# Optimization experiments

Measured on AMD Instinct MI355X. Metric: run time of the kernel, lower is better.

## Reference

```python
import jax, jax.numpy as jnp
import numpy as np

IN_SHAPE_DOWN = (8, 16, 8)   # prod = 1024
OUT_SHAPE_DOWN = (4, 4, 4)   # prod = 64
TT_RANK = 8


def tt_to_dense(cores, in_shape, out_shape):
    """Contract TT-matrix cores [r_{k-1}, i_k, j_k, r_k] into a dense (prod_in, prod_out) matrix."""
    res = cores[0]  # [1, i1, j1, r1]
    for c in cores[1:]:
        res = jnp.einsum('...a,aijb->...ijb', res, c)
    res = res[0, ..., 0]  # (i1, j1, i2, j2, ..., id, jd)
    d = len(in_shape)
    perm = [2 * k for k in range(d)] + [2 * k + 1 for k in range(d)]
    return res.transpose(perm).reshape(int(np.prod(in_shape)), int(np.prod(out_shape)))


def setup_inputs() -> dict:
    key = jax.random.key(0)
    ks = jax.random.split(key, 8)
    r = TT_RANK
    # down cores: in factors (8,16,8) -> out factors (4,4,4)
    d1 = 0.1 * jax.random.normal(ks[0], (1, 8, 4, r), dtype=jnp.float32)
    d2 = 0.1 * jax.random.normal(ks[1], (r, 16, 4, r), dtype=jnp.float32)
    d3 = 0.1 * jax.random.normal(ks[2], (r, 8, 4, 1), dtype=jnp.float32)
    # up cores: shape = [reversed(out_down), reversed(in_down)] = [(4,4,4),(8,16,8)]
    u1 = 0.1 * jax.random.normal(ks[3], (1, 4, 8, r), dtype=jnp.float32)
    u2 = 0.1 * jax.random.normal(ks[4], (r, 4, 16, r), dtype=jnp.float32)
    u3 = 0.1 * jax.random.normal(ks[5], (r, 4, 8, 1), dtype=jnp.float32)
    x = jax.random.normal(ks[6], (4, 4096, 1024), dtype=jnp.float32)
    bias_down = 0.001 * jnp.ones((64,), dtype=jnp.float32)
    bias_up = 0.001 * jnp.ones((1024,), dtype=jnp.float32)
    return {"x": x, "d1": d1, "d2": d2, "d3": d3,
            "u1": u1, "u2": u2, "u3": u3,
            "bias_down": bias_down, "bias_up": bias_up}


def reference(x, d1, d2, d3, u1, u2, u3, bias_down, bias_up):
    # Down-project TT matrix: 1024 -> 64
    Wd = tt_to_dense([d1, d2, d3], IN_SHAPE_DOWN, OUT_SHAPE_DOWN)
    # Up-project TT matrix: 64 -> 1024 (reversed factor shapes)
    Wu = tt_to_dense([u1, u2, u3], tuple(reversed(OUT_SHAPE_DOWN)), tuple(reversed(IN_SHAPE_DOWN)))
    z = jnp.einsum('bsd,dk->bsk', x, Wd) + bias_down
    z = jax.nn.relu(z)
    y = jnp.einsum('bsk,kd->bsd', z, Wu) + bias_up
    return y
```

## Files before the change

kernel.cpp:

```cpp
#include <hip/hip_runtime.h>

typedef float f32x2 __attribute__((ext_vector_type(2)));
typedef float f32x4 __attribute__((ext_vector_type(4)));
typedef short short8 __attribute__((ext_vector_type(8)));

static __device__ __forceinline__ unsigned short f2bf(float f) {
    __bf16 h = (__bf16)f;
    return __builtin_bit_cast(unsigned short, h);
}

static __device__ __forceinline__ void gload_lds16(const void* g, void* l) {
    __builtin_amdgcn_global_load_lds(
        (const __attribute__((address_space(1))) void*)g,
        (__attribute__((address_space(3))) void*)l, 16, 0, 0);
}

__global__ __launch_bounds__(256) void tt_build_w_kernel(
    const float* __restrict__ d1, const float* __restrict__ d2, const float* __restrict__ d3,
    const float* __restrict__ u1, const float* __restrict__ u2, const float* __restrict__ u3,
    unsigned short* __restrict__ WdT_sw, unsigned short* __restrict__ WuT_sw)
{
    int t = blockIdx.x * 256 + threadIdx.x;
    if (t < 65536) {
        int j = t >> 10, i = t & 1023;
        int i1 = i >> 7, i2 = (i >> 3) & 15, i3 = i & 7;
        int j1 = j >> 4, j2 = (j >> 2) & 3, j3 = j & 3;
        float t3[8];
#pragma unroll
        for (int b = 0; b < 8; ++b) t3[b] = d3[(b * 8 + i3) * 4 + j3];
        float wsum = 0.f;
#pragma unroll
        for (int a = 0; a < 8; ++a) {
            float va = d1[(i1 * 4 + j1) * 8 + a];
            const float* p2 = d2 + ((a * 16 + i2) * 4 + j2) * 8;
            float wa = 0.f;
#pragma unroll
            for (int b = 0; b < 8; ++b) wa = fmaf(p2[b], t3[b], wa);
            wsum = fmaf(va, wa, wsum);
        }
        int q_ = i >> 8, ck = (i >> 6) & 3, ks2 = (i >> 5) & 1;
        int kg_ = (i >> 3) & 3, m = i & 7;
        int off = (q_ * 4 + ck) * 4096 + ((ks2 * 4 + kg_) * 64 + j) * 8 + m;
        WdT_sw[off] = f2bf(wsum);
    } else {
        int t2 = t - 65536;
        int d = t2 >> 6, k = t2 & 63;
        int k1 = k >> 4, k2 = (k >> 2) & 3, k3 = k & 3;
        int o1 = d >> 7, o2 = (d >> 3) & 15, o3 = d & 7;
        float t3[8];
#pragma unroll
        for (int b = 0; b < 8; ++b) t3[b] = u3[(b * 4 + k3) * 8 + o3];
        float wsum = 0.f;
#pragma unroll
        for (int a = 0; a < 8; ++a) {
            float va = u1[(k1 * 8 + o1) * 8 + a];
            const float* p2 = u2 + ((a * 4 + k2) * 16 + o2) * 8;
            float wa = 0.f;
#pragma unroll
            for (int b = 0; b < 8; ++b) wa = fmaf(p2[b], t3[b], wa);
            wsum = fmaf(va, wa, wsum);
        }
        int dl = d & 511, hf = d >> 9;
        int off = hf * 32768 + (dl * 8 + ((k >> 3) ^ (dl & 7))) * 8 + (k & 7);
        WuT_sw[off] = f2bf(wsum);
    }
}

__global__ __launch_bounds__(512) void tt_gemm1_kernel(
    const float* __restrict__ x, const unsigned short* __restrict__ WdT_sw,
    const float* __restrict__ bd, unsigned short* __restrict__ zbuf)
{
    extern __shared__ unsigned short wlds[];
    const int t = threadIdx.x;
    const int lane = t & 63;
    const int w = t >> 6;
    const int p = w >> 2;
    const int h = w & 3;
    const int l15 = lane & 15;
    const int kg = lane >> 4;
    const int tile0 = blockIdx.x * 4;

    const int uq = (t & 127) * 2;
    const int tl = t >> 7;
    const int colz = (uq >> 6) * 16 + (uq & 15);
    const int rowz = ((uq & 63) >> 4) * 4;
    const f32x2 bdv = *reinterpret_cast<const f32x2*>(bd + colz);

    {
        const unsigned short* src = WdT_sw + (h * 4 + 2 * p) * 4096 + lane * 8;
        unsigned short* dst = wlds + h * 16384 + 2 * p * 4096;
#pragma unroll
        for (int i = 0; i < 16; ++i)
            gload_lds16(src + i * 512, dst + i * 512);
    }

    const float* xp0 = x + ((size_t)(tile0 + 2 * p) * 16 + l15) * 1024 + h * 256 + kg * 8;
    const float* xp1 = xp0 + 16 * 1024;
    const unsigned short* lb = wlds + h * 16384;

    f32x4 xa[8], xb[8];
#define XL8(D, o0, o1, o2, o3)                                                                     \
    asm volatile("global_load_dwordx4 %0, %1, off offset:" #o0 : "=v"(D[0]) : "v"(xp0) : "memory"); \
    asm volatile("global_load_dwordx4 %0, %1, off offset:" #o1 : "=v"(D[1]) : "v"(xp0) : "memory"); \
    asm volatile("global_load_dwordx4 %0, %1, off offset:" #o2 : "=v"(D[2]) : "v"(xp0) : "memory"); \
    asm volatile("global_load_dwordx4 %0, %1, off offset:" #o3 : "=v"(D[3]) : "v"(xp0) : "memory"); \
    asm volatile("global_load_dwordx4 %0, %1, off offset:" #o0 : "=v"(D[4]) : "v"(xp1) : "memory"); \
    asm volatile("global_load_dwordx4 %0, %1, off offset:" #o1 : "=v"(D[5]) : "v"(xp1) : "memory"); \
    asm volatile("global_load_dwordx4 %0, %1, off offset:" #o2 : "=v"(D[6]) : "v"(xp1) : "memory"); \
    asm volatile("global_load_dwordx4 %0, %1, off offset:" #o3 : "=v"(D[7]) : "v"(xp1) : "memory");

    XL8(xa, 0, 16, 128, 144)
    asm volatile("s_waitcnt vmcnt(8)" ::: "memory");
    __syncthreads();

    f32x4 acc0[4] = {{0.f, 0.f, 0.f, 0.f}, {0.f, 0.f, 0.f, 0.f},
                     {0.f, 0.f, 0.f, 0.f}, {0.f, 0.f, 0.f, 0.f}};
    f32x4 acc1[4] = {{0.f, 0.f, 0.f, 0.f}, {0.f, 0.f, 0.f, 0.f},
                     {0.f, 0.f, 0.f, 0.f}, {0.f, 0.f, 0.f, 0.f}};

#define CPT(XS, CKOFF, WN) do {                                                             \
    asm volatile("s_waitcnt vmcnt(" #WN ")" ::: "memory");                                  \
    __builtin_amdgcn_sched_barrier(0);                                                      \
    const unsigned short* lb_ = lb + CKOFF;                                                 \
    _Pragma("unroll")                                                                       \
    for (int ks2 = 0; ks2 < 2; ++ks2) {                                                     \
        union { short8 v; unsigned short e[8]; } a0, a1;                                    \
        _Pragma("unroll")                                                                   \
        for (int e = 0; e < 4; ++e) {                                                       \
            a0.e[e] = f2bf(XS[ks2 * 2][e]);     a0.e[e + 4] = f2bf(XS[ks2 * 2 + 1][e]);     \
            a1.e[e] = f2bf(XS[4 + ks2 * 2][e]); a1.e[e + 4] = f2bf(XS[4 + ks2 * 2 + 1][e]); \
        }                                                                                   \
        _Pragma("unroll")                                                                   \
        for (int ct = 0; ct < 4; ++ct) {                                                    \
            short8 bf = *reinterpret_cast<const short8*>(                                   \
                lb_ + (ks2 * 4 + kg) * 512 + ct * 128 + l15 * 8);                           \
            acc0[ct] = __builtin_amdgcn_mfma_f32_16x16x32_bf16(a0.v, bf, acc0[ct], 0, 0, 0); \
            acc1[ct] = __builtin_amdgcn_mfma_f32_16x16x32_bf16(a1.v, bf, acc1[ct], 0, 0, 0); \
        }                                                                                   \
    }                                                                                       \
    __builtin_amdgcn_sched_barrier(0);                                                      \
} while (0)

    XL8(xb, 256, 272, 384, 400)
    CPT(xa, 0, 8);
    XL8(xa, 512, 528, 640, 656)
    CPT(xb, 4096, 8);
    XL8(xb, 768, 784, 896, 912)
    CPT(xa, 8192, 8);
    CPT(xb, 12288, 0);
#undef XL8
#undef CPT

    __syncthreads();

    float* red = reinterpret_cast<float*>(wlds);
    {
        float* rp = red + p * 8192 + h * 2048;
#pragma unroll
        for (int ct = 0; ct < 4; ++ct) {
            *reinterpret_cast<f32x4*>(rp + ct * 256 + lane * 4) = acc0[ct];
            *reinterpret_cast<f32x4*>(rp + 1024 + ct * 256 + lane * 4) = acc1[ct];
        }
    }
    __syncthreads();

    {
        const int pp = tl >> 1, tp = tl & 1;
        const float* base = red + pp * 8192 + tp * 1024 + uq * 4;
        f32x4 s0 = {0.f, 0.f, 0.f, 0.f}, s1 = {0.f, 0.f, 0.f, 0.f};
#pragma unroll
        for (int hh = 0; hh < 4; ++hh) {
            f32x4 v0 = *reinterpret_cast<const f32x4*>(base + hh * 2048);
            f32x4 v1 = *reinterpret_cast<const f32x4*>(base + hh * 2048 + 4);
#pragma unroll
            for (int r = 0; r < 4; ++r) { s0[r] += v0[r]; s1[r] += v1[r]; }
        }
        const int tile = tile0 + tl;
#pragma unroll
        for (int r = 0; r < 4; ++r) {
            float z0 = s0[r] + bdv[0]; z0 = z0 > 0.f ? z0 : 0.f;
            float z1 = s1[r] + bdv[1]; z1 = z1 > 0.f ? z1 : 0.f;
            unsigned int pk = (unsigned int)f2bf(z0) | ((unsigned int)f2bf(z1) << 16);
            *reinterpret_cast<unsigned int*>(zbuf + tile * 1024 + (rowz + r) * 64 + colz) = pk;
        }
    }
}

__global__ __launch_bounds__(256) void tt_gemm2_kernel(
    const unsigned short* __restrict__ zbuf, const unsigned short* __restrict__ WuT_sw,
    const float* __restrict__ bu, float* __restrict__ y)
{
    __shared__ unsigned short wlds2[32768];
    const int t = threadIdx.x;
    const int lane = t & 63;
    const int w = t >> 6;
    const int l15 = lane & 15;
    const int kg = lane >> 4;
    const int ch = blockIdx.x & 1;
    const int rg = blockIdx.x >> 1;

    const unsigned short* src = WuT_sw + ch * 32768 + w * 8192 + lane * 8;
#pragma unroll
    for (int i = 0; i < 16; ++i)
        gload_lds16(src + i * 512, &wlds2[w * 8192 + i * 512]);

    f32x4 bv[8];
#pragma unroll
    for (int i = 0; i < 8; ++i)
        bv[i] = *reinterpret_cast<const f32x4*>(bu + ch * 512 + w * 128 + i * 16 + kg * 4);
    __syncthreads();

#pragma unroll
    for (int tt = 0; tt < 8; ++tt) {
        const int tile = rg * 8 + tt;
        short8 az0 = *reinterpret_cast<const short8*>(zbuf + tile * 1024 + l15 * 64 + kg * 8);
        short8 az1 = *reinterpret_cast<const short8*>(zbuf + tile * 1024 + l15 * 64 + 32 + kg * 8);
        const size_t yb = (size_t)(tile * 16 + l15) * 1024 + ch * 512 + w * 128;
#pragma unroll
        for (int i = 0; i < 8; ++i) {
            const int row = w * 128 + i * 16 + l15;
            const int s = row & 7;
            short8 b0 = *reinterpret_cast<const short8*>(&wlds2[(row * 8 + (kg ^ s)) * 8]);
            short8 b1 = *reinterpret_cast<const short8*>(&wlds2[(row * 8 + ((kg + 4) ^ s)) * 8]);
            f32x4 c = {0.f, 0.f, 0.f, 0.f};
            c = __builtin_amdgcn_mfma_f32_16x16x32_bf16(b0, az0, c, 0, 0, 0);
            c = __builtin_amdgcn_mfma_f32_16x16x32_bf16(b1, az1, c, 0, 0, 0);
            f32x4 o;
#pragma unroll
            for (int r = 0; r < 4; ++r) o[r] = c[r] + bv[i][r];
            *reinterpret_cast<f32x4*>(y + yb + i * 16 + kg * 4) = o;
        }
    }
}

extern "C" void kernel_launch(void* const* d_in, const int* in_sizes, int n_in,
                              void* d_out, int out_size, void* d_ws, size_t ws_size,
                              hipStream_t stream) {
    const float* x  = (const float*)d_in[0];
    const float* d1 = (const float*)d_in[1];
    const float* d2 = (const float*)d_in[2];
    const float* d3 = (const float*)d_in[3];
    const float* u1 = (const float*)d_in[4];
    const float* u2 = (const float*)d_in[5];
    const float* u3 = (const float*)d_in[6];
    const float* bd = (const float*)d_in[7];
    const float* bu = (const float*)d_in[8];
    float* y = (float*)d_out;
    unsigned short* WdT_sw = (unsigned short*)d_ws;
    unsigned short* WuT_sw = WdT_sw + 65536;
    unsigned short* zbuf   = WuT_sw + 65536;

    hipLaunchKernelGGL(tt_build_w_kernel, dim3(512), dim3(256), 0, stream,
                       d1, d2, d3, u1, u2, u3, WdT_sw, WuT_sw);
    hipLaunchKernelGGL(tt_gemm1_kernel, dim3(256), dim3(512), 131072, stream,
                       x, WdT_sw, bd, zbuf);
    hipLaunchKernelGGL(tt_gemm2_kernel, dim3(256), dim3(256), 0, stream,
                       zbuf, WuT_sw, bu, y);
}
```

Measured before the change: 37.75 us.

## Load down-projection weights directly into registers and halve gemm1 block size

The first GEMM kernel drops its 128KB LDS staging of the bf16 down weights. Each wave now loads its weight fragments straight from global memory into registers, double-buffered alongside the x loads. The block shrinks to 256 threads, with each wave handling 4 row tiles of 16 rows over one K quarter, and only a 64KB static LDS buffer is kept for the cross-wave reduction. This is meant to cut LDS traffic and the upfront LDS fill barrier and to allow more blocks per CU. The cost is redundant global or L2 weight reads per wave, more accumulator registers, and unpacked 2-byte z stores.

```diff
diff --git a/kernel.cpp b/kernel.cpp
--- a/kernel.cpp
+++ b/kernel.cpp
@@ -66,122 +66,108 @@
     }
 }
 
-__global__ __launch_bounds__(512) void tt_gemm1_kernel(
+__global__ __launch_bounds__(256) void tt_gemm1_kernel(
     const float* __restrict__ x, const unsigned short* __restrict__ WdT_sw,
     const float* __restrict__ bd, unsigned short* __restrict__ zbuf)
 {
-    extern __shared__ unsigned short wlds[];
+    __shared__ float red[4][4][1024];
     const int t = threadIdx.x;
     const int lane = t & 63;
-    const int w = t >> 6;
-    const int p = w >> 2;
-    const int h = w & 3;
+    const int h = t >> 6;
     const int l15 = lane & 15;
     const int kg = lane >> 4;
     const int tile0 = blockIdx.x * 4;
 
-    const int uq = (t & 127) * 2;
-    const int tl = t >> 7;
-    const int colz = (uq >> 6) * 16 + (uq & 15);
-    const int rowz = ((uq & 63) >> 4) * 4;
-    const f32x2 bdv = *reinterpret_cast<const f32x2*>(bd + colz);
-
-    {
-        const unsigned short* src = WdT_sw + (h * 4 + 2 * p) * 4096 + lane * 8;
-        unsigned short* dst = wlds + h * 16384 + 2 * p * 4096;
-#pragma unroll
-        for (int i = 0; i < 16; ++i)
-            gload_lds16(src + i * 512, dst + i * 512);
-    }
-
-    const float* xp0 = x + ((size_t)(tile0 + 2 * p) * 16 + l15) * 1024 + h * 256 + kg * 8;
+    const int colz = (t >> 6) * 16 + (t & 15);
+    const int rowz = ((t & 63) >> 4) * 4;
+    const float bdv = bd[colz];
+
+    const float* xp0 = x + ((size_t)(tile0 + 0) * 16 + l15) * 1024 + h * 256 + kg * 8;
     const float* xp1 = xp0 + 16 * 1024;
-    const unsigned short* lb = wlds + h * 16384;
-
-    f32x4 xa[8], xb[8];
-#define XL8(D, o0, o1, o2, o3)                                                                     \
-    asm volatile("global_load_dwordx4 %0, %1, off offset:" #o0 : "=v"(D[0]) : "v"(xp0) : "memory"); \
-    asm volatile("global_load_dwordx4 %0, %1, off offset:" #o1 : "=v"(D[1]) : "v"(xp0) : "memory"); \
-    asm volatile("global_load_dwordx4 %0, %1, off offset:" #o2 : "=v"(D[2]) : "v"(xp0) : "memory"); \
-    asm volatile("global_load_dwordx4 %0, %1, off offset:" #o3 : "=v"(D[3]) : "v"(xp0) : "memory"); \
-    asm volatile("global_load_dwordx4 %0, %1, off offset:" #o0 : "=v"(D[4]) : "v"(xp1) : "memory"); \
-    asm volatile("global_load_dwordx4 %0, %1, off offset:" #o1 : "=v"(D[5]) : "v"(xp1) : "memory"); \
-    asm volatile("global_load_dwordx4 %0, %1, off offset:" #o2 : "=v"(D[6]) : "v"(xp1) : "memory"); \
-    asm volatile("global_load_dwordx4 %0, %1, off offset:" #o3 : "=v"(D[7]) : "v"(xp1) : "memory");
-
-    XL8(xa, 0, 16, 128, 144)
-    asm volatile("s_waitcnt vmcnt(8)" ::: "memory");
+    const float* xp2 = xp0 + 32 * 1024;
+    const float* xp3 = xp0 + 48 * 1024;
+    const unsigned short* wqb = WdT_sw + h * 16384 + kg * 512 + l15 * 8;
+    const unsigned short* wq0 = wqb;
+    const unsigned short* wq1 = wqb + 2048;
+    const unsigned short* wq2 = wqb + 4096;
+    const unsigned short* wq3 = wqb + 6144;
+    const unsigned short* wq4 = wqb + 8192;
+    const unsigned short* wq5 = wqb + 10240;
+    const unsigned short* wq6 = wqb + 12288;
+    const unsigned short* wq7 = wqb + 14336;
+
+    f32x4 xA[8], xB[8];
+    short8 wA[4], wB[4];
+    f32x4 acc[4][4];
+#pragma unroll
+    for (int t4 = 0; t4 < 4; ++t4)
+#pragma unroll
+        for (int ct = 0; ct < 4; ++ct) acc[t4][ct] = {0.f, 0.f, 0.f, 0.f};
+
+#define ISSUE(D, W, WQ, O0, O1)                                                                   \
+    asm volatile("global_load_dwordx4 %0, %1, off offset:" #O0 : "=v"(D[0]) : "v"(xp0) : "memory"); \
+    asm volatile("global_load_dwordx4 %0, %1, off offset:" #O1 : "=v"(D[1]) : "v"(xp0) : "memory"); \
+    asm volatile("global_load_dwordx4 %0, %1, off offset:" #O0 : "=v"(D[2]) : "v"(xp1) : "memory"); \
+    asm volatile("global_load_dwordx4 %0, %1, off offset:" #O1 : "=v"(D[3]) : "v"(xp1) : "memory"); \
+    asm volatile("global_load_dwordx4 %0, %1, off offset:" #O0 : "=v"(D[4]) : "v"(xp2) : "memory"); \
+    asm volatile("global_load_dwordx4 %0, %1, off offset:" #O1 : "=v"(D[5]) : "v"(xp2) : "memory"); \
+    asm volatile("global_load_dwordx4 %0, %1, off offset:" #O0 : "=v"(D[6]) : "v"(xp3) : "memory"); \
+    asm volatile("global_load_dwordx4 %0, %1, off offset:" #O1 : "=v"(D[7]) : "v"(xp3) : "memory"); \
+    asm volatile("global_load_dwordx4 %0, %1, off offset:0"   : "=v"(W[0]) : "v"(WQ) : "memory");   \
+    asm volatile("global_load_dwordx4 %0, %1, off offset:256" : "=v"(W[1]) : "v"(WQ) : "memory");   \
+    asm volatile("global_load_dwordx4 %0, %1, off offset:512" : "=v"(W[2]) : "v"(WQ) : "memory");   \
+    asm volatile("global_load_dwordx4 %0, %1, off offset:768" : "=v"(W[3]) : "v"(WQ) : "memory");
+
+#define CPT(D, W, WN) do {                                                                   \
+    asm volatile("s_waitcnt vmcnt(" #WN ")" ::: "memory");                                   \
+    __builtin_amdgcn_sched_barrier(0);                                                       \
+    _Pragma("unroll")                                                                        \
+    for (int t4 = 0; t4 < 4; ++t4) {                                                         \
+        union { short8 v; unsigned short e[8]; } a;                                          \
+        _Pragma("unroll")                                                                    \
+        for (int e = 0; e < 4; ++e) {                                                        \
+            a.e[e]     = f2bf(D[2 * t4][e]);                                                 \
+            a.e[e + 4] = f2bf(D[2 * t4 + 1][e]);                                             \
+        }                                                                                    \
+        _Pragma("unroll")                                                                    \
+        for (int ct = 0; ct < 4; ++ct)                                                       \
+            acc[t4][ct] = __builtin_amdgcn_mfma_f32_16x16x32_bf16(a.v, W[ct], acc[t4][ct],   \
+                                                                  0, 0, 0);                  \
+    }                                                                                        \
+    __builtin_amdgcn_sched_barrier(0);                                                       \
+} while (0)
+
+    ISSUE(xA, wA, wq0, 0, 16)
+    ISSUE(xB, wB, wq1, 128, 144)
+    CPT(xA, wA, 12); ISSUE(xA, wA, wq2, 256, 272)
+    CPT(xB, wB, 12); ISSUE(xB, wB, wq3, 384, 400)
+    CPT(xA, wA, 12); ISSUE(xA, wA, wq4, 512, 528)
+    CPT(xB, wB, 12); ISSUE(xB, wB, wq5, 640, 656)
+    CPT(xA, wA, 12); ISSUE(xA, wA, wq6, 768, 784)
+    CPT(xB, wB, 12); ISSUE(xB, wB, wq7, 896, 912)
+    CPT(xA, wA, 12);
+    CPT(xB, wB, 0);
+#undef ISSUE
+#undef CPT
+
+#pragma unroll
+    for (int t4 = 0; t4 < 4; ++t4)
+#pragma unroll
+        for (int ct = 0; ct < 4; ++ct)
+            *reinterpret_cast<f32x4*>(&red[t4][h][ct * 256 + lane * 4]) = acc[t4][ct];
     __syncthreads();
-
-    f32x4 acc0[4] = {{0.f, 0.f, 0.f, 0.f}, {0.f, 0.f, 0.f, 0.f},
-                     {0.f, 0.f, 0.f, 0.f}, {0.f, 0.f, 0.f, 0.f}};
-    f32x4 acc1[4] = {{0.f, 0.f, 0.f, 0.f}, {0.f, 0.f, 0.f, 0.f},
-                     {0.f, 0.f, 0.f, 0.f}, {0.f, 0.f, 0.f, 0.f}};
-
-#define CPT(XS, CKOFF, WN) do {                                                             \
-    asm volatile("s_waitcnt vmcnt(" #WN ")" ::: "memory");                                  \
-    __builtin_amdgcn_sched_barrier(0);                                                      \
-    const unsigned short* lb_ = lb + CKOFF;                                                 \
-    _Pragma("unroll")                                                                       \
-    for (int ks2 = 0; ks2 < 2; ++ks2) {                                                     \
-        union { short8 v; unsigned short e[8]; } a0, a1;                                    \
-        _Pragma("unroll")                                                                   \
-        for (int e = 0; e < 4; ++e) {                                                       \
-            a0.e[e] = f2bf(XS[ks2 * 2][e]);     a0.e[e + 4] = f2bf(XS[ks2 * 2 + 1][e]);     \
-            a1.e[e] = f2bf(XS[4 + ks2 * 2][e]); a1.e[e + 4] = f2bf(XS[4 + ks2 * 2 + 1][e]); \
-        }                                                                                   \
-        _Pragma("unroll")                                                                   \
-        for (int ct = 0; ct < 4; ++ct) {                                                    \
-            short8 bf = *reinterpret_cast<const short8*>(                                   \
-                lb_ + (ks2 * 4 + kg) * 512 + ct * 128 + l15 * 8);                           \
-            acc0[ct] = __builtin_amdgcn_mfma_f32_16x16x32_bf16(a0.v, bf, acc0[ct], 0, 0, 0); \
-            acc1[ct] = __builtin_amdgcn_mfma_f32_16x16x32_bf16(a1.v, bf, acc1[ct], 0, 0, 0); \
-        }                                                                                   \
-    }                                                                                       \
-    __builtin_amdgcn_sched_barrier(0);                                                      \
-} while (0)
-
-    XL8(xb, 256, 272, 384, 400)
-    CPT(xa, 0, 8);
-    XL8(xa, 512, 528, 640, 656)
-    CPT(xb, 4096, 8);
-    XL8(xb, 768, 784, 896, 912)
-    CPT(xa, 8192, 8);
-    CPT(xb, 12288, 0);
-#undef XL8
-#undef CPT
-
-    __syncthreads();
-
-    float* red = reinterpret_cast<float*>(wlds);
-    {
-        float* rp = red + p * 8192 + h * 2048;
-#pragma unroll
-        for (int ct = 0; ct < 4; ++ct) {
-            *reinterpret_cast<f32x4*>(rp + ct * 256 + lane * 4) = acc0[ct];
-            *reinterpret_cast<f32x4*>(rp + 1024 + ct * 256 + lane * 4) = acc1[ct];
-        }
-    }
-    __syncthreads();
-
-    {
-        const int pp = tl >> 1, tp = tl & 1;
-        const float* base = red + pp * 8192 + tp * 1024 + uq * 4;
-        f32x4 s0 = {0.f, 0.f, 0.f, 0.f}, s1 = {0.f, 0.f, 0.f, 0.f};
-#pragma unroll
-        for (int hh = 0; hh < 4; ++hh) {
-            f32x4 v0 = *reinterpret_cast<const f32x4*>(base + hh * 2048);
-            f32x4 v1 = *reinterpret_cast<const f32x4*>(base + hh * 2048 + 4);
-#pragma unroll
-            for (int r = 0; r < 4; ++r) { s0[r] += v0[r]; s1[r] += v1[r]; }
-        }
-        const int tile = tile0 + tl;
+#pragma unroll
+    for (int t4 = 0; t4 < 4; ++t4) {
+        f32x4 v0 = *reinterpret_cast<const f32x4*>(&red[t4][0][t * 4]);
+        f32x4 v1 = *reinterpret_cast<const f32x4*>(&red[t4][1][t * 4]);
+        f32x4 v2 = *reinterpret_cast<const f32x4*>(&red[t4][2][t * 4]);
+        f32x4 v3 = *reinterpret_cast<const f32x4*>(&red[t4][3][t * 4]);
+        const int tile = tile0 + t4;
 #pragma unroll
         for (int r = 0; r < 4; ++r) {
-            float z0 = s0[r] + bdv[0]; z0 = z0 > 0.f ? z0 : 0.f;
-            float z1 = s1[r] + bdv[1]; z1 = z1 > 0.f ? z1 : 0.f;
-            unsigned int pk = (unsigned int)f2bf(z0) | ((unsigned int)f2bf(z1) << 16);
-            *reinterpret_cast<unsigned int*>(zbuf + tile * 1024 + (rowz + r) * 64 + colz) = pk;
+            float zz = v0[r] + v1[r] + v2[r] + v3[r] + bdv;
+            zz = zz > 0.f ? zz : 0.f;
+            zbuf[tile * 1024 + (rowz + r) * 64 + colz] = f2bf(zz);
         }
     }
 }
@@ -252,7 +238,7 @@
 
     hipLaunchKernelGGL(tt_build_w_kernel, dim3(512), dim3(256), 0, stream,
                        d1, d2, d3, u1, u2, u3, WdT_sw, WuT_sw);
-    hipLaunchKernelGGL(tt_gemm1_kernel, dim3(256), dim3(512), 131072, stream,
+    hipLaunchKernelGGL(tt_gemm1_kernel, dim3(256), dim3(256), 0, stream,
                        x, WdT_sw, bd, zbuf);
     hipLaunchKernelGGL(tt_gemm2_kernel, dim3(256), dim3(256), 0, stream,
                        zbuf, WuT_sw, bu, y);
```

New measurement: 35.76 us. 5.3% less time.
